# Kernel tuning notes

Measured on AMD Instinct MI355X. Metric: run time of the kernel, lower is better.

The kernel has to match this reference:

```python
import jax, jax.numpy as jnp
import numpy as np

N, E, R = 50000, 1600000, 8
IN_F, HID_F, OUT_F = 128, 64, 64


def setup_inputs() -> dict:
    key = jax.random.key(0)
    ks = jax.random.split(key, 9)
    x = jax.random.normal(ks[0], (N, IN_F), dtype=jnp.float32)
    edge_index = jax.random.randint(ks[1], (2, E), 0, N, dtype=jnp.int64)
    edge_type = jax.random.randint(ks[2], (E,), 0, R, dtype=jnp.int64)
    # layer 1 params (scaled like glorot)
    s1 = 1.0 / np.sqrt(IN_F)
    W1_rel = jax.random.normal(ks[3], (R, IN_F, HID_F), dtype=jnp.float32) * s1
    W1_root = jax.random.normal(ks[4], (IN_F, HID_F), dtype=jnp.float32) * s1
    b1 = jnp.zeros((HID_F,), dtype=jnp.float32)
    # layer 2 params
    s2 = 1.0 / np.sqrt(HID_F)
    W2_rel = jax.random.normal(ks[5], (R, HID_F, OUT_F), dtype=jnp.float32) * s2
    W2_root = jax.random.normal(ks[6], (HID_F, OUT_F), dtype=jnp.float32) * s2
    b2 = jnp.zeros((OUT_F,), dtype=jnp.float32)
    return {"x": x, "edge_index": edge_index, "edge_type": edge_type,
            "W1_rel": W1_rel, "W1_root": W1_root, "b1": b1,
            "W2_rel": W2_rel, "W2_root": W2_root, "b2": b2}


def _rgcn_conv(x, src, dst, etype, W_rel, W_root, b):
    """PyG RGCNConv: root transform + per-relation mean-aggregated messages."""
    n = x.shape[0]
    r = W_rel.shape[0]
    # per-relation transform of all node features: [R, N, H]
    xw = jnp.einsum('nd,rdh->rnh', x, W_rel)
    # per-edge message: transformed source feature under the edge's relation
    msg = xw[etype, src]  # [E, H]
    # mean normalization per (dst, relation) pair
    key = dst * r + etype  # [E]
    cnt = jax.ops.segment_sum(jnp.ones(etype.shape, dtype=x.dtype), key,
                              num_segments=n * r)
    inv = 1.0 / jnp.maximum(cnt, 1.0)
    msg = msg * inv[key][:, None]
    # scatter-add into target nodes
    agg = jax.ops.segment_sum(msg, dst, num_segments=n)  # [N, H]
    return agg + x @ W_root + b


def reference(x, edge_index, edge_type, W1_rel, W1_root, b1, W2_rel, W2_root, b2):
    src, dst = edge_index[0], edge_index[1]
    h = _rgcn_conv(x, src, dst, edge_type, W1_rel, W1_root, b1)
    h = jax.nn.relu(h)
    out = _rgcn_conv(h, src, dst, edge_type, W2_rel, W2_root, b2)
    return out
```

## Files before the change

kernel.cpp:

```cpp
#include <hip/hip_runtime.h>


constexpr int NN  = 50000;
constexpr int NE  = 1600000;
constexpr int NR  = 8;
constexpr int FIN = 128;
constexpr int FH  = 64;

constexpr int BSH = 7;
constexpr int BN  = 1 << BSH;
constexpr int NB  = (NN + BN - 1) >> BSH;
constexpr int CAP = 6144;
constexpr int CH  = 8192;
constexpr unsigned XWMAX = (unsigned)(NN - 1) * (NR * 64) + (NR - 1) * 64;

typedef __attribute__((ext_vector_type(8))) short bf16x8;
typedef __attribute__((ext_vector_type(4))) float f32x4;

__device__ __forceinline__ unsigned short f2bf(float f) {
  unsigned u = __float_as_uint(f);
  u = (u + 0x7fff + ((u >> 16) & 1)) >> 16;
  return (unsigned short)u;
}
__device__ __forceinline__ float bf2f(unsigned short b) {
  return __uint_as_float(((unsigned)b) << 16);
}
__device__ __forceinline__ bool edge_ok(unsigned s, unsigned d, unsigned r) {
  return s < NN && d < NN && r < NR;
}

__global__ void bcur_init(int* __restrict__ bcur) {
  const int i = blockIdx.x * blockDim.x + threadIdx.x;
  if (i < NB) bcur[i] = i * CAP;
}

__global__ void __launch_bounds__(256) bucket_append(
    const int* __restrict__ src, const int* __restrict__ dst,
    const int* __restrict__ et, int* __restrict__ bcur,
    uint2* __restrict__ brecs) {
  __shared__ uint2 stage[CH];
  __shared__ int h[NB], gbase[NB], sbase[NB], scur[NB];
  __shared__ int wtot[4];
  const int t  = threadIdx.x;
  const int c0 = blockIdx.x * CH;
  const int m  = min(CH, NE - c0);

  for (int i = t; i < NB; i += 256) h[i] = 0;
  __syncthreads();

  for (int i = t; i < m; i += 256) {
    const unsigned s = (unsigned)src[c0 + i];
    const unsigned d = (unsigned)dst[c0 + i];
    const unsigned r = (unsigned)et[c0 + i];
    if (edge_ok(s, d, r)) atomicAdd(&h[d >> BSH], 1);
  }
  __syncthreads();

  const int v0 = (2 * t < NB) ? h[2 * t] : 0;
  const int v1 = (2 * t + 1 < NB) ? h[2 * t + 1] : 0;
  if (2 * t < NB     && v0) gbase[2 * t]     = atomicAdd(&bcur[2 * t], v0);
  if (2 * t + 1 < NB && v1) gbase[2 * t + 1] = atomicAdd(&bcur[2 * t + 1], v1);
  const int s = v0 + v1;
  int incl = s;
#pragma unroll
  for (int o = 1; o < 64; o <<= 1) {
    int u = __shfl_up(incl, o, 64);
    if ((t & 63) >= o) incl += u;
  }
  if ((t & 63) == 63) wtot[t >> 6] = incl;
  __syncthreads();
  int wo = 0;
  for (int w = 0; w < (t >> 6); ++w) wo += wtot[w];
  const int e = wo + incl - s;
  if (2 * t < NB)     { sbase[2 * t] = e;          scur[2 * t] = e; }
  if (2 * t + 1 < NB) { sbase[2 * t + 1] = e + v0; scur[2 * t + 1] = e + v0; }
  __syncthreads();

  for (int i = t; i < m; i += 256) {
    const unsigned sv = (unsigned)src[c0 + i];
    const unsigned d  = (unsigned)dst[c0 + i];
    const unsigned r  = (unsigned)et[c0 + i];
    if (edge_ok(sv, d, r)) {
      const int p = atomicAdd(&scur[d >> BSH], 1);
      if (p < CH) stage[p] = make_uint2((sv << 9) | (r << 6), d);
    }
  }
  __syncthreads();

  const int M = min(sbase[NB - 1] + h[NB - 1], CH);
  for (int j = t; j < M; j += 256) {
    const uint2 rec = stage[j];
    const int b = (int)(rec.y >> BSH);
    const int idx = min(gbase[b] + (j - sbase[b]), NB * CAP - 1);
    brecs[idx] = rec;
  }
}

__global__ void __launch_bounds__(256) bucket_finalize(
    const int* __restrict__ bcur, const uint2* __restrict__ brecs,
    float* __restrict__ inv, int* __restrict__ row_start,
    int* __restrict__ deg, unsigned* __restrict__ recs) {
  const int b    = blockIdx.x;
  const int base = b * CAP;
  const int m    = min(bcur[b] - base, CAP);
  const int d0   = b << BSH;
  __shared__ int cnt[BN * NR];
  __shared__ int curs[BN * NR];
  __shared__ int wtot[4];
  const int t = threadIdx.x;

  for (int i = t; i < BN * NR; i += 256) cnt[i] = 0;
  __syncthreads();
  for (int i = t; i < m; i += 256) {
    const uint2 rec = brecs[base + i];
    const int dl = (int)(rec.y & (BN - 1));
    const int r  = (rec.x >> 6) & 7;
    atomicAdd(&cnt[dl * NR + r], 1);
  }
  __syncthreads();

  const int c0 = cnt[t * 4], c1 = cnt[t * 4 + 1], c2 = cnt[t * 4 + 2], c3 = cnt[t * 4 + 3];
  const int s = c0 + c1 + c2 + c3;
  int incl = s;
#pragma unroll
  for (int o = 1; o < 64; o <<= 1) {
    int u = __shfl_up(incl, o, 64);
    if ((t & 63) >= o) incl += u;
  }
  if ((t & 63) == 63) wtot[t >> 6] = incl;
  __syncthreads();
  int wo = 0;
  for (int w = 0; w < (t >> 6); ++w) wo += wtot[w];
  const int e = wo + incl - s;
  curs[t * 4]     = e;
  curs[t * 4 + 1] = e + c0;
  curs[t * 4 + 2] = e + c0 + c1;
  curs[t * 4 + 3] = e + c0 + c1 + c2;
  __syncthreads();

  if (t < BN) {
    const int d = d0 + t;
    if (d < NN) {
      const int start = curs[t * NR];
      const int end   = (t == BN - 1) ? m : curs[(t + 1) * NR];
      row_start[d] = base + start;
      deg[d]       = end - start;
#pragma unroll
      for (int r = 0; r < NR; ++r)
        inv[d * NR + r] = 1.0f / fmaxf((float)cnt[t * NR + r], 1.0f);
    }
  }
  __syncthreads();

  for (int i = t; i < m; i += 256) {
    const uint2 rec = brecs[base + i];
    const int dl = (int)(rec.y & (BN - 1));
    const int r  = (rec.x >> 6) & 7;
    const int p  = atomicAdd(&curs[dl * NR + r], 1);
    recs[base + min(p, CAP - 1)] = rec.x;
  }
}

__global__ void cvt_w_all(const float* __restrict__ W1r, const float* __restrict__ W1o,
                          const float* __restrict__ W2r, const float* __restrict__ W2o,
                          unsigned short* __restrict__ Wt1,
                          unsigned short* __restrict__ Wt2) {
  const int i  = blockIdx.x * blockDim.x + threadIdx.x;
  const int n1 = (NR + 1) * 64 * FIN;
  const int n2 = (NR + 1) * 64 * FH;
  if (i < n1) {
    const int g = i / (64 * FIN), rem = i % (64 * FIN);
    const int n = rem / FIN, k = rem % FIN;
    const float* W = (g < NR) ? (W1r + (size_t)g * FIN * 64) : W1o;
    Wt1[i] = f2bf(W[k * 64 + n]);
  } else if (i < n1 + n2) {
    const int j = i - n1;
    const int g = j / (64 * FH), rem = j % (64 * FH);
    const int n = rem / FH, k = rem % FH;
    const float* W = (g < NR) ? (W2r + (size_t)g * FH * 64) : W2o;
    Wt2[j] = f2bf(W[k * 64 + n]);
  }
}

template <int K, bool A_FP32>
__global__ void __launch_bounds__(256) gemm_mfma(
    const void* __restrict__ Av, const unsigned short* __restrict__ Wt,
    const float* __restrict__ bias,
    unsigned short* __restrict__ xw, float* __restrict__ root_out) {
  constexpr int KP  = K + 8;
  constexpr int NCH = 64 * (K / 8) / 256;
  __shared__ unsigned short As[64 * KP];
  __shared__ unsigned short Bs[2][64 * KP];
  const int n0  = blockIdx.x * 64;
  const int tid = threadIdx.x;

  if constexpr (A_FP32) {
    const float* A = (const float*)Av;
    for (int c = tid; c < 64 * (K / 8); c += 256) {
      const int row = c / (K / 8), kp = (c % (K / 8)) * 8;
      bf16x8 v = {};
      if (n0 + row < NN) {
        const float* p = A + (size_t)(n0 + row) * K + kp;
        const float4 f0 = *(const float4*)p;
        const float4 f1 = *(const float4*)(p + 4);
        v[0] = f2bf(f0.x); v[1] = f2bf(f0.y); v[2] = f2bf(f0.z); v[3] = f2bf(f0.w);
        v[4] = f2bf(f1.x); v[5] = f2bf(f1.y); v[6] = f2bf(f1.z); v[7] = f2bf(f1.w);
      }
      *(bf16x8*)(As + row * KP + kp) = v;
    }
  } else {
    const unsigned short* A = (const unsigned short*)Av;
    for (int c = tid; c < 64 * (K / 8); c += 256) {
      const int row = c / (K / 8), kp = (c % (K / 8)) * 8;
      bf16x8 v = {};
      if (n0 + row < NN) v = *(const bf16x8*)(A + (size_t)(n0 + row) * K + kp);
      *(bf16x8*)(As + row * KP + kp) = v;
    }
  }

  for (int c = 0; c < NCH; ++c) {
    const int idx = tid + c * 256;
    const int row = idx / (K / 8), kp = (idx % (K / 8)) * 8;
    *(bf16x8*)(Bs[0] + row * KP + kp) = *(const bf16x8*)(Wt + idx * 8);
  }
  __syncthreads();

  const int wave = tid >> 6, lane = tid & 63;
  const int i16 = lane & 15, quad = lane >> 4;
  const int r0 = wave * 16 + i16;

  for (int g = 0; g <= NR; ++g) {
    const int buf = g & 1;
    bf16x8 breg[NCH];
    if (g < NR) {
      const unsigned short* Wn = Wt + (size_t)(g + 1) * 64 * K;
#pragma unroll
      for (int c = 0; c < NCH; ++c) breg[c] = *(const bf16x8*)(Wn + (tid + c * 256) * 8);
    }

    f32x4 acc[4] = {};
#pragma unroll
    for (int kc = 0; kc < K / 32; ++kc) {
      const int k0 = kc * 32 + quad * 8;
      const bf16x8 a0 = *(const bf16x8*)(As + r0 * KP + k0);
      const bf16x8 b0 = *(const bf16x8*)(Bs[buf] + (i16)      * KP + k0);
      const bf16x8 b1 = *(const bf16x8*)(Bs[buf] + (i16 + 16) * KP + k0);
      const bf16x8 b2 = *(const bf16x8*)(Bs[buf] + (i16 + 32) * KP + k0);
      const bf16x8 b3 = *(const bf16x8*)(Bs[buf] + (i16 + 48) * KP + k0);
      acc[0] = __builtin_amdgcn_mfma_f32_16x16x32_bf16(a0, b0, acc[0], 0, 0, 0);
      acc[1] = __builtin_amdgcn_mfma_f32_16x16x32_bf16(a0, b1, acc[1], 0, 0, 0);
      acc[2] = __builtin_amdgcn_mfma_f32_16x16x32_bf16(a0, b2, acc[2], 0, 0, 0);
      acc[3] = __builtin_amdgcn_mfma_f32_16x16x32_bf16(a0, b3, acc[3], 0, 0, 0);
    }

    if (g < NR) {
#pragma unroll
      for (int c = 0; c < NCH; ++c) {
        const int idx = tid + c * 256;
        const int row = idx / (K / 8), kp = (idx % (K / 8)) * 8;
        *(bf16x8*)(Bs[buf ^ 1] + row * KP + kp) = breg[c];
      }
    }

    if (g < NR) {
#pragma unroll
      for (int reg = 0; reg < 4; ++reg) {
        const int n = n0 + wave * 16 + quad * 4 + reg;
        if (n >= NN) continue;
        unsigned short* p = xw + (size_t)n * (NR * 64) + g * 64 + i16;
#pragma unroll
        for (int ct = 0; ct < 4; ++ct) p[ct * 16] = f2bf(acc[ct][reg]);
      }
    } else {
      float bv[4];
#pragma unroll
      for (int ct = 0; ct < 4; ++ct) bv[ct] = bias[ct * 16 + i16];
#pragma unroll
      for (int reg = 0; reg < 4; ++reg) {
        const int n = n0 + wave * 16 + quad * 4 + reg;
        if (n >= NN) continue;
        float* p = root_out + (size_t)n * 64 + i16;
#pragma unroll
        for (int ct = 0; ct < 4; ++ct) p[ct * 16] = acc[ct][reg] + bv[ct];
      }
    }
    __syncthreads();
  }
}

template <bool RELU_BF16>
__global__ void __launch_bounds__(256) agg_csr(
    const int* __restrict__ row_start, const int* __restrict__ deg,
    const unsigned* __restrict__ offs, const unsigned short* __restrict__ xw,
    const float* __restrict__ inv, const float* __restrict__ root,
    float* __restrict__ out_f32, unsigned short* __restrict__ out_b16) {
  const int gid  = blockIdx.x * blockDim.x + threadIdx.x;
  const int lane = gid & 63;
  const int d    = gid >> 6;
  if (d >= NN) return;
  const int e  = lane >> 3;
  const int l8 = lane & 7;
  const int base = row_start[d];
  const int n    = deg[d];
  const float invv = inv[(d << 3) + l8];
  float a[8] = {};

  for (int c = 0; c < n; c += 64) {
    const int m = min(64, n - c);
    unsigned off = 0;
    if (lane < m) off = offs[base + c + lane];
    for (int j = 0; j < m; j += 16) {
      const int i0 = j + e, i1 = j + 8 + e;
      unsigned u0 = __shfl(off, i0 & 63, 64);
      unsigned u1 = __shfl(off, i1 & 63, 64);
      float s0 = __shfl(invv, (int)((u0 >> 6) & 7), 64);
      float s1 = __shfl(invv, (int)((u1 >> 6) & 7), 64);
      u0 = min(u0, XWMAX); u1 = min(u1, XWMAX);
      if (i0 >= m) s0 = 0.f;
      if (i1 >= m) s1 = 0.f;
      const bf16x8 v0 = *(const bf16x8*)(xw + u0 + l8 * 8);
      const bf16x8 v1 = *(const bf16x8*)(xw + u1 + l8 * 8);
#pragma unroll
      for (int q = 0; q < 8; ++q) a[q] += bf2f((unsigned short)v0[q]) * s0;
#pragma unroll
      for (int q = 0; q < 8; ++q) a[q] += bf2f((unsigned short)v1[q]) * s1;
    }
  }

#pragma unroll
  for (int q = 0; q < 8; ++q) {
    a[q] += __shfl_xor(a[q], 8, 64);
    a[q] += __shfl_xor(a[q], 16, 64);
    a[q] += __shfl_xor(a[q], 32, 64);
  }

  if (e == 0) {
    const float4 r0 = *(const float4*)(root + (size_t)d * 64 + l8 * 8);
    const float4 r1 = *(const float4*)(root + (size_t)d * 64 + l8 * 8 + 4);
    const float o[8] = {r0.x + a[0], r0.y + a[1], r0.z + a[2], r0.w + a[3],
                        r1.x + a[4], r1.y + a[5], r1.z + a[6], r1.w + a[7]};
    if (RELU_BF16) {
      bf16x8 ov;
#pragma unroll
      for (int q = 0; q < 8; ++q) ov[q] = (short)f2bf(fmaxf(o[q], 0.f));
      *(bf16x8*)(out_b16 + (size_t)d * 64 + l8 * 8) = ov;
    } else {
      *(float4*)(out_f32 + (size_t)d * 64 + l8 * 8)     = make_float4(o[0], o[1], o[2], o[3]);
      *(float4*)(out_f32 + (size_t)d * 64 + l8 * 8 + 4) = make_float4(o[4], o[5], o[6], o[7]);
    }
  }
}

extern "C" void kernel_launch(void* const* d_in, const int* in_sizes, int n_in,
                              void* d_out, int out_size, void* d_ws, size_t ws_size,
                              hipStream_t stream) {
  const float* x   = (const float*)d_in[0];
  const int*   ei  = (const int*)d_in[1];
  const int*   et  = (const int*)d_in[2];
  const float* W1r = (const float*)d_in[3];
  const float* W1o = (const float*)d_in[4];
  const float* b1  = (const float*)d_in[5];
  const float* W2r = (const float*)d_in[6];
  const float* W2o = (const float*)d_in[7];
  const float* b2  = (const float*)d_in[8];
  float* out = (float*)d_out;

  const int* src = ei;
  const int* dst = ei + NE;

  char* ws = (char*)d_ws;
  size_t off = 0;
  auto alloc = [&](size_t bytes) {
    void* p = ws + off; off += (bytes + 255) & ~(size_t)255; return p;
  };
  int*   bcur      = (int*)alloc((size_t)NB * 4);
  float* inv       = (float*)alloc((size_t)NN * NR * 4);
  int*   row_start = (int*)alloc((size_t)NN * 4);
  int*   deg       = (int*)alloc((size_t)NN * 4);
  uint2* brecs     = (uint2*)alloc((size_t)NB * CAP * 8);
  unsigned* offs   = (unsigned*)alloc((size_t)NB * CAP * 4);
  unsigned short* xw    = (unsigned short*)alloc((size_t)NN * NR * 64 * 2);
  unsigned short* hb    = (unsigned short*)alloc((size_t)NN * FH * 2);
  float*          hroot = (float*)alloc((size_t)NN * 64 * 4);
  unsigned short* Wt1   = (unsigned short*)alloc((size_t)(NR + 1) * 64 * FIN * 2);
  unsigned short* Wt2   = (unsigned short*)alloc((size_t)(NR + 1) * 64 * FH * 2);

  bcur_init<<<(NB + 255) / 256, 256, 0, stream>>>(bcur);
  bucket_append<<<(NE + CH - 1) / CH, 256, 0, stream>>>(src, dst, et, bcur, brecs);
  bucket_finalize<<<NB, 256, 0, stream>>>(bcur, brecs, inv, row_start, deg, offs);

  const int ncvt = (NR + 1) * 64 * (FIN + FH);
  cvt_w_all<<<(ncvt + 255) / 256, 256, 0, stream>>>(W1r, W1o, W2r, W2o, Wt1, Wt2);

  const int gemm_blocks = (NN + 63) / 64;
  const int agg_blocks  = (NN * 64 + 255) / 256;
  gemm_mfma<FIN, true><<<gemm_blocks, 256, 0, stream>>>(x, Wt1, b1, xw, hroot);
  agg_csr<true><<<agg_blocks, 256, 0, stream>>>(row_start, deg, offs, xw, inv, hroot, nullptr, hb);
  gemm_mfma<FH, false><<<gemm_blocks, 256, 0, stream>>>(hb, Wt2, b2, xw, out);
  agg_csr<false><<<agg_blocks, 256, 0, stream>>>(row_start, deg, offs, xw, inv, out, out, nullptr);
}
```

Measured before the change: 254.0 us.

## Aggregate raw features per relation before transform and fuse each layer

Reorders each RGCN layer to aggregate first and transform second. Source node features are summed per (dst, relation) into shared memory, then one MFMA GEMM runs over the concatenated [R+1]*K inputs with bias and ReLU fused in the epilogue. This removes the large per-relation xw intermediate (N*R*64 bf16) and the separate root buffer, and replaces two GEMM kernels plus two gather kernels with two fused kernels. In exchange, the gather is serial per edge within a wave and reads K_IN-wide rows (128 for layer 1), and it relies on the record order grouping edges by relation.

```diff
diff --git a/kernel.cpp b/kernel.cpp
--- a/kernel.cpp
+++ b/kernel.cpp
@@ -12,7 +12,6 @@
 constexpr int NB  = (NN + BN - 1) >> BSH;
 constexpr int CAP = 6144;
 constexpr int CH  = 8192;
-constexpr unsigned XWMAX = (unsigned)(NN - 1) * (NR * 64) + (NR - 1) * 64;
 
 typedef __attribute__((ext_vector_type(8))) short bf16x8;
 typedef __attribute__((ext_vector_type(4))) float f32x4;
@@ -161,20 +160,29 @@
   }
 }
 
-__global__ void cvt_w_all(const float* __restrict__ W1r, const float* __restrict__ W1o,
-                          const float* __restrict__ W2r, const float* __restrict__ W2o,
-                          unsigned short* __restrict__ Wt1,
-                          unsigned short* __restrict__ Wt2) {
-  const int i  = blockIdx.x * blockDim.x + threadIdx.x;
-  const int n1 = (NR + 1) * 64 * FIN;
-  const int n2 = (NR + 1) * 64 * FH;
-  if (i < n1) {
-    const int g = i / (64 * FIN), rem = i % (64 * FIN);
+__global__ void prep(const float* __restrict__ x,
+                     const float* __restrict__ W1r, const float* __restrict__ W1o,
+                     const float* __restrict__ W2r, const float* __restrict__ W2o,
+                     unsigned short* __restrict__ xb,
+                     unsigned short* __restrict__ Wt1,
+                     unsigned short* __restrict__ Wt2) {
+  const int i   = blockIdx.x * blockDim.x + threadIdx.x;
+  const int NX  = NN * FIN / 4;
+  const int NW1 = (NR + 1) * 64 * FIN;
+  const int NW2 = (NR + 1) * 64 * FH;
+  if (i < NX) {
+    const float4 v = ((const float4*)x)[i];
+    ushort4 o;
+    o.x = f2bf(v.x); o.y = f2bf(v.y); o.z = f2bf(v.z); o.w = f2bf(v.w);
+    ((ushort4*)xb)[i] = o;
+  } else if (i < NX + NW1) {
+    const int j = i - NX;
+    const int g = j / (64 * FIN), rem = j % (64 * FIN);
     const int n = rem / FIN, k = rem % FIN;
     const float* W = (g < NR) ? (W1r + (size_t)g * FIN * 64) : W1o;
-    Wt1[i] = f2bf(W[k * 64 + n]);
-  } else if (i < n1 + n2) {
-    const int j = i - n1;
+    Wt1[j] = f2bf(W[k * 64 + n]);
+  } else if (i < NX + NW1 + NW2) {
+    const int j = i - NX - NW1;
     const int g = j / (64 * FH), rem = j % (64 * FH);
     const int n = rem / FH, k = rem % FH;
     const float* W = (g < NR) ? (W2r + (size_t)g * FH * 64) : W2o;
@@ -182,171 +190,112 @@
   }
 }
 
-template <int K, bool A_FP32>
-__global__ void __launch_bounds__(256) gemm_mfma(
-    const void* __restrict__ Av, const unsigned short* __restrict__ Wt,
+template <int K_IN, int MTILE, bool RELU_BF16>
+__global__ void __launch_bounds__(256) fused_layer(
+    const int* __restrict__ row_start, const int* __restrict__ deg,
+    const unsigned* __restrict__ offs, const float* __restrict__ inv,
+    const unsigned short* __restrict__ fin,
+    const unsigned short* __restrict__ Wt,
     const float* __restrict__ bias,
-    unsigned short* __restrict__ xw, float* __restrict__ root_out) {
-  constexpr int KP  = K + 8;
-  constexpr int NCH = 64 * (K / 8) / 256;
-  __shared__ unsigned short As[64 * KP];
-  __shared__ unsigned short Bs[2][64 * KP];
-  const int n0  = blockIdx.x * 64;
+    unsigned short* __restrict__ out_b16, float* __restrict__ out_f32) {
+  constexpr int SROW = (NR + 1) * K_IN + 8;
+  __shared__ unsigned short S[MTILE * SROW];
+  const int n0  = blockIdx.x * MTILE;
   const int tid = threadIdx.x;
-
-  if constexpr (A_FP32) {
-    const float* A = (const float*)Av;
-    for (int c = tid; c < 64 * (K / 8); c += 256) {
-      const int row = c / (K / 8), kp = (c % (K / 8)) * 8;
-      bf16x8 v = {};
-      if (n0 + row < NN) {
-        const float* p = A + (size_t)(n0 + row) * K + kp;
-        const float4 f0 = *(const float4*)p;
-        const float4 f1 = *(const float4*)(p + 4);
-        v[0] = f2bf(f0.x); v[1] = f2bf(f0.y); v[2] = f2bf(f0.z); v[3] = f2bf(f0.w);
-        v[4] = f2bf(f1.x); v[5] = f2bf(f1.y); v[6] = f2bf(f1.z); v[7] = f2bf(f1.w);
+  const int wave = tid >> 6, lane = tid & 63;
+
+  for (int i = tid * 8; i < MTILE * SROW; i += 2048)
+    *(bf16x8*)(S + i) = (bf16x8){};
+  __syncthreads();
+
+  for (int i = tid; i < MTILE * (K_IN / 8); i += 256) {
+    const int dl = i / (K_IN / 8), kp = (i % (K_IN / 8)) * 8;
+    const int d = n0 + dl;
+    bf16x8 v = {};
+    if (d < NN) v = *(const bf16x8*)(fin + (size_t)d * K_IN + kp);
+    *(bf16x8*)(S + dl * SROW + NR * K_IN + kp) = v;
+  }
+
+  for (int dl = wave; dl < MTILE; dl += 4) {
+    const int d = n0 + dl;
+    if (d >= NN) break;
+    const int base = row_start[d];
+    const int n    = deg[d];
+    unsigned short* Srow = S + dl * SROW;
+    float a0 = 0.f, a1 = 0.f;
+    int cur = -1;
+    for (int c = 0; c < n; c += 64) {
+      const int m = min(64, n - c);
+      unsigned rec = 0;
+      if (lane < m) rec = offs[base + c + lane];
+      for (int j = 0; j < m; ++j) {
+        const unsigned u  = __shfl(rec, j, 64);
+        const int      r  = (int)((u >> 6) & 7);
+        const unsigned sv = u >> 9;
+        if (r != cur) {
+          if (cur >= 0) {
+            const float sc = inv[(d << 3) + cur];
+            if constexpr (K_IN == 128) {
+              const unsigned pk = ((unsigned)f2bf(a1 * sc) << 16) | f2bf(a0 * sc);
+              *(unsigned*)(Srow + cur * K_IN + lane * 2) = pk;
+            } else {
+              Srow[cur * K_IN + lane] = f2bf(a0 * sc);
+            }
+          }
+          cur = r; a0 = 0.f; a1 = 0.f;
+        }
+        if constexpr (K_IN == 128) {
+          const unsigned v = *(const unsigned*)(fin + (size_t)sv * K_IN + lane * 2);
+          a0 += bf2f((unsigned short)(v & 0xffffu));
+          a1 += bf2f((unsigned short)(v >> 16));
+        } else {
+          a0 += bf2f(fin[(size_t)sv * K_IN + lane]);
+        }
       }
-      *(bf16x8*)(As + row * KP + kp) = v;
-    }
-  } else {
-    const unsigned short* A = (const unsigned short*)Av;
-    for (int c = tid; c < 64 * (K / 8); c += 256) {
-      const int row = c / (K / 8), kp = (c % (K / 8)) * 8;
-      bf16x8 v = {};
-      if (n0 + row < NN) v = *(const bf16x8*)(A + (size_t)(n0 + row) * K + kp);
-      *(bf16x8*)(As + row * KP + kp) = v;
-    }
-  }
-
-  for (int c = 0; c < NCH; ++c) {
-    const int idx = tid + c * 256;
-    const int row = idx / (K / 8), kp = (idx % (K / 8)) * 8;
-    *(bf16x8*)(Bs[0] + row * KP + kp) = *(const bf16x8*)(Wt + idx * 8);
-  }
-  __syncthreads();
-
-  const int wave = tid >> 6, lane = tid & 63;
+    }
+    if (cur >= 0) {
+      const float sc = inv[(d << 3) + cur];
+      if constexpr (K_IN == 128) {
+        const unsigned pk = ((unsigned)f2bf(a1 * sc) << 16) | f2bf(a0 * sc);
+        *(unsigned*)(Srow + cur * K_IN + lane * 2) = pk;
+      } else {
+        Srow[cur * K_IN + lane] = f2bf(a0 * sc);
+      }
+    }
+  }
+  __syncthreads();
+
   const int i16 = lane & 15, quad = lane >> 4;
-  const int r0 = wave * 16 + i16;
-
+  constexpr int MT = MTILE / 16;
+  f32x4 acc[MT] = {};
+#pragma unroll
   for (int g = 0; g <= NR; ++g) {
-    const int buf = g & 1;
-    bf16x8 breg[NCH];
-    if (g < NR) {
-      const unsigned short* Wn = Wt + (size_t)(g + 1) * 64 * K;
-#pragma unroll
-      for (int c = 0; c < NCH; ++c) breg[c] = *(const bf16x8*)(Wn + (tid + c * 256) * 8);
-    }
-
-    f32x4 acc[4] = {};
-#pragma unroll
-    for (int kc = 0; kc < K / 32; ++kc) {
-      const int k0 = kc * 32 + quad * 8;
-      const bf16x8 a0 = *(const bf16x8*)(As + r0 * KP + k0);
-      const bf16x8 b0 = *(const bf16x8*)(Bs[buf] + (i16)      * KP + k0);
-      const bf16x8 b1 = *(const bf16x8*)(Bs[buf] + (i16 + 16) * KP + k0);
-      const bf16x8 b2 = *(const bf16x8*)(Bs[buf] + (i16 + 32) * KP + k0);
-      const bf16x8 b3 = *(const bf16x8*)(Bs[buf] + (i16 + 48) * KP + k0);
-      acc[0] = __builtin_amdgcn_mfma_f32_16x16x32_bf16(a0, b0, acc[0], 0, 0, 0);
-      acc[1] = __builtin_amdgcn_mfma_f32_16x16x32_bf16(a0, b1, acc[1], 0, 0, 0);
-      acc[2] = __builtin_amdgcn_mfma_f32_16x16x32_bf16(a0, b2, acc[2], 0, 0, 0);
-      acc[3] = __builtin_amdgcn_mfma_f32_16x16x32_bf16(a0, b3, acc[3], 0, 0, 0);
-    }
-
-    if (g < NR) {
-#pragma unroll
-      for (int c = 0; c < NCH; ++c) {
-        const int idx = tid + c * 256;
-        const int row = idx / (K / 8), kp = (idx % (K / 8)) * 8;
-        *(bf16x8*)(Bs[buf ^ 1] + row * KP + kp) = breg[c];
+#pragma unroll
+    for (int kc = 0; kc < K_IN / 32; ++kc) {
+      const int ko = g * K_IN + kc * 32 + quad * 8;
+      const bf16x8 b = *(const bf16x8*)(
+          Wt + (size_t)(g * 64 + wave * 16 + i16) * K_IN + kc * 32 + quad * 8);
+#pragma unroll
+      for (int mt = 0; mt < MT; ++mt) {
+        const bf16x8 a = *(const bf16x8*)(S + (mt * 16 + i16) * SROW + ko);
+        acc[mt] = __builtin_amdgcn_mfma_f32_16x16x32_bf16(a, b, acc[mt], 0, 0, 0);
       }
     }
-
-    if (g < NR) {
-#pragma unroll
-      for (int reg = 0; reg < 4; ++reg) {
-        const int n = n0 + wave * 16 + quad * 4 + reg;
-        if (n >= NN) continue;
-        unsigned short* p = xw + (size_t)n * (NR * 64) + g * 64 + i16;
-#pragma unroll
-        for (int ct = 0; ct < 4; ++ct) p[ct * 16] = f2bf(acc[ct][reg]);
-      }
-    } else {
-      float bv[4];
-#pragma unroll
-      for (int ct = 0; ct < 4; ++ct) bv[ct] = bias[ct * 16 + i16];
-#pragma unroll
-      for (int reg = 0; reg < 4; ++reg) {
-        const int n = n0 + wave * 16 + quad * 4 + reg;
-        if (n >= NN) continue;
-        float* p = root_out + (size_t)n * 64 + i16;
-#pragma unroll
-        for (int ct = 0; ct < 4; ++ct) p[ct * 16] = acc[ct][reg] + bv[ct];
-      }
-    }
-    __syncthreads();
-  }
-}
-
-template <bool RELU_BF16>
-__global__ void __launch_bounds__(256) agg_csr(
-    const int* __restrict__ row_start, const int* __restrict__ deg,
-    const unsigned* __restrict__ offs, const unsigned short* __restrict__ xw,
-    const float* __restrict__ inv, const float* __restrict__ root,
-    float* __restrict__ out_f32, unsigned short* __restrict__ out_b16) {
-  const int gid  = blockIdx.x * blockDim.x + threadIdx.x;
-  const int lane = gid & 63;
-  const int d    = gid >> 6;
-  if (d >= NN) return;
-  const int e  = lane >> 3;
-  const int l8 = lane & 7;
-  const int base = row_start[d];
-  const int n    = deg[d];
-  const float invv = inv[(d << 3) + l8];
-  float a[8] = {};
-
-  for (int c = 0; c < n; c += 64) {
-    const int m = min(64, n - c);
-    unsigned off = 0;
-    if (lane < m) off = offs[base + c + lane];
-    for (int j = 0; j < m; j += 16) {
-      const int i0 = j + e, i1 = j + 8 + e;
-      unsigned u0 = __shfl(off, i0 & 63, 64);
-      unsigned u1 = __shfl(off, i1 & 63, 64);
-      float s0 = __shfl(invv, (int)((u0 >> 6) & 7), 64);
-      float s1 = __shfl(invv, (int)((u1 >> 6) & 7), 64);
-      u0 = min(u0, XWMAX); u1 = min(u1, XWMAX);
-      if (i0 >= m) s0 = 0.f;
-      if (i1 >= m) s1 = 0.f;
-      const bf16x8 v0 = *(const bf16x8*)(xw + u0 + l8 * 8);
-      const bf16x8 v1 = *(const bf16x8*)(xw + u1 + l8 * 8);
-#pragma unroll
-      for (int q = 0; q < 8; ++q) a[q] += bf2f((unsigned short)v0[q]) * s0;
-#pragma unroll
-      for (int q = 0; q < 8; ++q) a[q] += bf2f((unsigned short)v1[q]) * s1;
-    }
-  }
-
-#pragma unroll
-  for (int q = 0; q < 8; ++q) {
-    a[q] += __shfl_xor(a[q], 8, 64);
-    a[q] += __shfl_xor(a[q], 16, 64);
-    a[q] += __shfl_xor(a[q], 32, 64);
-  }
-
-  if (e == 0) {
-    const float4 r0 = *(const float4*)(root + (size_t)d * 64 + l8 * 8);
-    const float4 r1 = *(const float4*)(root + (size_t)d * 64 + l8 * 8 + 4);
-    const float o[8] = {r0.x + a[0], r0.y + a[1], r0.z + a[2], r0.w + a[3],
-                        r1.x + a[4], r1.y + a[5], r1.z + a[6], r1.w + a[7]};
-    if (RELU_BF16) {
-      bf16x8 ov;
-#pragma unroll
-      for (int q = 0; q < 8; ++q) ov[q] = (short)f2bf(fmaxf(o[q], 0.f));
-      *(bf16x8*)(out_b16 + (size_t)d * 64 + l8 * 8) = ov;
-    } else {
-      *(float4*)(out_f32 + (size_t)d * 64 + l8 * 8)     = make_float4(o[0], o[1], o[2], o[3]);
-      *(float4*)(out_f32 + (size_t)d * 64 + l8 * 8 + 4) = make_float4(o[4], o[5], o[6], o[7]);
+  }
+
+  const int col = wave * 16 + i16;
+  const float bv = bias[col];
+#pragma unroll
+  for (int mt = 0; mt < MT; ++mt) {
+#pragma unroll
+    for (int reg = 0; reg < 4; ++reg) {
+      const int d = n0 + mt * 16 + quad * 4 + reg;
+      if (d >= NN) continue;
+      const float h = acc[mt][reg] + bv;
+      if constexpr (RELU_BF16)
+        out_b16[(size_t)d * 64 + col] = f2bf(fmaxf(h, 0.f));
+      else
+        out_f32[(size_t)d * 64 + col] = h;
     }
   }
 }
@@ -379,23 +328,20 @@
   int*   deg       = (int*)alloc((size_t)NN * 4);
   uint2* brecs     = (uint2*)alloc((size_t)NB * CAP * 8);
   unsigned* offs   = (unsigned*)alloc((size_t)NB * CAP * 4);
-  unsigned short* xw    = (unsigned short*)alloc((size_t)NN * NR * 64 * 2);
-  unsigned short* hb    = (unsigned short*)alloc((size_t)NN * FH * 2);
-  float*          hroot = (float*)alloc((size_t)NN * 64 * 4);
-  unsigned short* Wt1   = (unsigned short*)alloc((size_t)(NR + 1) * 64 * FIN * 2);
-  unsigned short* Wt2   = (unsigned short*)alloc((size_t)(NR + 1) * 64 * FH * 2);
+  unsigned short* xb  = (unsigned short*)alloc((size_t)NN * FIN * 2);
+  unsigned short* hb  = (unsigned short*)alloc((size_t)NN * FH * 2);
+  unsigned short* Wt1 = (unsigned short*)alloc((size_t)(NR + 1) * 64 * FIN * 2);
+  unsigned short* Wt2 = (unsigned short*)alloc((size_t)(NR + 1) * 64 * FH * 2);
 
   bcur_init<<<(NB + 255) / 256, 256, 0, stream>>>(bcur);
   bucket_append<<<(NE + CH - 1) / CH, 256, 0, stream>>>(src, dst, et, bcur, brecs);
   bucket_finalize<<<NB, 256, 0, stream>>>(bcur, brecs, inv, row_start, deg, offs);
 
-  const int ncvt = (NR + 1) * 64 * (FIN + FH);
-  cvt_w_all<<<(ncvt + 255) / 256, 256, 0, stream>>>(W1r, W1o, W2r, W2o, Wt1, Wt2);
-
-  const int gemm_blocks = (NN + 63) / 64;
-  const int agg_blocks  = (NN * 64 + 255) / 256;
-  gemm_mfma<FIN, true><<<gemm_blocks, 256, 0, stream>>>(x, Wt1, b1, xw, hroot);
-  agg_csr<true><<<agg_blocks, 256, 0, stream>>>(row_start, deg, offs, xw, inv, hroot, nullptr, hb);
-  gemm_mfma<FH, false><<<gemm_blocks, 256, 0, stream>>>(hb, Wt2, b2, xw, out);
-  agg_csr<false><<<agg_blocks, 256, 0, stream>>>(row_start, deg, offs, xw, inv, out, out, nullptr);
-}
+  const int nprep = NN * FIN / 4 + (NR + 1) * 64 * (FIN + FH);
+  prep<<<(nprep + 255) / 256, 256, 0, stream>>>(x, W1r, W1o, W2r, W2o, xb, Wt1, Wt2);
+
+  fused_layer<FIN, 16, true><<<(NN + 15) / 16, 256, 0, stream>>>(
+      row_start, deg, offs, inv, xb, Wt1, b1, hb, nullptr);
+  fused_layer<FH, 32, false><<<(NN + 31) / 32, 256, 0, stream>>>(
+      row_start, deg, offs, inv, hb, Wt2, b2, nullptr, out);
+}
```

Measured after the change: 653.1 us. 157% more time.
